# Kernel tuning notes

Hardware: AMD Instinct MI355X
Metric: run time of the kernel (lower is better)

The kernel has to match this reference:

```python
import jax, jax.numpy as jnp
import numpy as np

RADIUS = 0.2
NSAMPLE = 32


def ball_query(radius, nsample, xyz, new_xyz):
    # xyz: (B, N, 3), new_xyz: (B, M, 3) -> idx: (B, M, nsample) int32
    N = xyz.shape[1]
    # squared distances (B, M, N)
    d2 = jnp.sum((new_xyz[:, :, None, :] - xyz[:, None, :, :]) ** 2, axis=-1)
    # key = point index if within radius else N (sentinel); take nsample smallest keys
    key = jnp.where(d2 < radius * radius, jnp.arange(N, dtype=jnp.int32), N)
    neg_top, _ = jax.lax.top_k(-key, nsample)  # ascending keys = earliest in-radius indices
    idx = -neg_top  # (B, M, nsample)
    valid = idx < N
    first = idx[..., :1]
    first = jnp.where(first < N, first, 0)  # if ball empty, fall back to index 0
    return jnp.where(valid, idx, first)


def group_points(features, idx):
    # features: (B, C, N), idx: (B, M, S) -> (B, C, M, S)
    return jax.vmap(lambda f, i: f[:, i])(features, idx)


def setup_inputs() -> dict:
    key = jax.random.key(0)
    k1, k2, k3 = jax.random.split(key, 3)
    B, N, M, C = 4, 16384, 2048, 64
    xyz = jax.random.uniform(k1, (B, N, 3), dtype=jnp.float32)
    new_xyz = jax.random.uniform(k2, (B, M, 3), dtype=jnp.float32)
    features = jax.random.normal(k3, (B, C, N), dtype=jnp.float32)
    return {"xyz": xyz, "new_xyz": new_xyz, "features": features}


def reference(xyz, new_xyz, features):
    idx = ball_query(RADIUS, NSAMPLE, xyz, new_xyz)  # (B, M, S)
    xyz_t = jnp.transpose(xyz, (0, 2, 1))  # (B, 3, N)
    grouped_xyz = group_points(xyz_t, idx)  # (B, 3, M, S)
    grouped_xyz = grouped_xyz - jnp.transpose(new_xyz, (0, 2, 1))[..., None]
    grouped_features = group_points(features, idx)  # (B, C, M, S)
    # use_xyz=True: concat relative coordinates with grouped features
    return jnp.concatenate([grouped_xyz, grouped_features], axis=1)  # (B, 3+C, M, S)
```

## Files before the change

kernel.cpp:

```cpp
#include <hip/hip_runtime.h>


#define WPB 4
constexpr int Bc = 4, Nc = 16384, Mc = 2048, Cc = 64, Sc = 32;

__global__ __launch_bounds__(256) void transpose_kernel(
    const float* __restrict__ feat,
    float* __restrict__ featT)
{
    __shared__ float tile[64][65];
    const int b = blockIdx.y;
    const int nbase = blockIdx.x * 64;
    const int tid = threadIdx.x;
    const int tn = tid & 63;
    const int tq = tid >> 6;
    const float* fb = feat + (size_t)b * Cc * Nc;
    float* ob = featT + (size_t)b * Nc * Cc;
    #pragma unroll
    for (int k = 0; k < 16; ++k) {
        const int c = k * 4 + tq;
        tile[tn][c] = fb[(size_t)c * Nc + nbase + tn];
    }
    __syncthreads();
    #pragma unroll
    for (int k = 0; k < 16; ++k) {
        const int nl = k * 4 + tq;
        ob[(size_t)(nbase + nl) * Cc + tn] = tile[nl][tn];
    }
}

__global__ __launch_bounds__(256) void qg_kernel(
    const float* __restrict__ xyz,
    const float* __restrict__ new_xyz,
    const float* __restrict__ feat,
    const float* __restrict__ featT,
    float* __restrict__ out,
    int useT)
{
#pragma clang fp contract(off)
    const int lane = threadIdx.x & 63;
    const int wv   = threadIdx.x >> 6;
    const int q    = blockIdx.x * WPB + wv;
    const int b    = q >> 11;
    const int m    = q & (Mc - 1);

    __shared__ int sidx[WPB][Sc];

    const float r2 = 0.2f * 0.2f;
    const float* nz = new_xyz + (size_t)(b * Mc + m) * 3;
    const float qx = nz[0], qy = nz[1], qz = nz[2];
    const float* xb = xyz + (size_t)b * Nc * 3;

    int count = 0, firstIdx = 0;
    const unsigned long long lt = (1ull << lane) - 1ull;
    for (int base = 0; base < Nc; base += 256) {
        float px[4], py[4], pz[4];
        #pragma unroll
        for (int u = 0; u < 4; ++u) {
            const float* pp = xb + (size_t)(base + u * 64 + lane) * 3;
            px[u] = pp[0]; py[u] = pp[1]; pz[u] = pp[2];
        }
        #pragma unroll
        for (int u = 0; u < 4; ++u) {
            const float dx = qx - px[u], dy = qy - py[u], dz = qz - pz[u];
            float d2 = dx * dx + dy * dy;
            d2 = d2 + dz * dz;
            const bool in = d2 < r2;
            const unsigned long long mask = __ballot(in);
            if (in) {
                const int slot = count + __popcll(mask & lt);
                if (slot < Sc) sidx[wv][slot] = base + u * 64 + lane;
            }
            if (count == 0 && mask != 0ull)
                firstIdx = base + u * 64 + __builtin_ctzll(mask);
            count += __popcll(mask);
        }
        if (count >= Sc) break;
    }
    {
        const int start = count < Sc ? count : Sc;
        if (start + lane < Sc) sidx[wv][start + lane] = firstIdx;
    }
    asm volatile("s_waitcnt lgkmcnt(0)" ::: "memory");

    const int s     = lane & 31;
    const int chalf = lane >> 5;
    const int myid  = sidx[wv][s];
    float* ob = out + ((size_t)b * 67 * Mc + m) * Sc;

    #pragma unroll
    for (int it = 0; it < 2; ++it) {
        const int c = it * 2 + chalf;
        if (c < 3) {
            const float ctr = (c == 0) ? qx : (c == 1) ? qy : qz;
            ob[(size_t)c * (Mc * Sc) + s] = xb[(size_t)myid * 3 + c] - ctr;
        }
    }

    if (useT) {
        const float* ftb = featT + ((size_t)b * Nc + myid) * Cc;
        #pragma unroll
        for (int it = 0; it < 8; ++it) {
            const int c4 = it * 2 + chalf;
            const float4 v = *(const float4*)(ftb + (size_t)c4 * 4);
            #pragma unroll
            for (int k = 0; k < 4; ++k)
                ob[(size_t)(3 + c4 * 4 + k) * (Mc * Sc) + s] = ((const float*)&v)[k];
        }
    } else {
        const float* fb = feat + (size_t)b * Cc * Nc;
        #pragma unroll
        for (int it = 0; it < 32; ++it) {
            const int c = it * 2 + chalf;
            ob[(size_t)(3 + c) * (Mc * Sc) + s] = fb[(size_t)c * Nc + myid];
        }
    }
}

extern "C" void kernel_launch(void* const* d_in, const int* in_sizes, int n_in,
                              void* d_out, int out_size, void* d_ws, size_t ws_size,
                              hipStream_t stream) {
    const float* xyz     = (const float*)d_in[0];
    const float* new_xyz = (const float*)d_in[1];
    const float* feat    = (const float*)d_in[2];
    float* out           = (float*)d_out;

    const size_t needT = (size_t)Bc * Nc * Cc * sizeof(float);
    float* featT = (float*)d_ws;
    const int useT = (ws_size >= needT) ? 1 : 0;

    if (useT) {
        dim3 g(Nc / 64, Bc);
        hipLaunchKernelGGL(transpose_kernel, g, dim3(256), 0, stream, feat, featT);
    }
    hipLaunchKernelGGL(qg_kernel, dim3((Bc * Mc) / WPB), dim3(256), 0, stream,
                       xyz, new_xyz, feat, featT, out, useT);
}
```

Before: 38.88 us.

## Overlap feature transpose with ball query in one prep kernel, then gather separately

Merges the feature transpose and the ball-query search into a single prep kernel, with different blocks handling each, so the two independent stages can run concurrently instead of back to back. Neighbor indices now go to a global workspace instead of shared memory, and a separate gather kernel reads them and writes the output from the transposed features. The cost is an extra kernel launch and a global round-trip for the index buffer. The shared-memory tile is also allocated in ball-query blocks, which may limit occupancy.

Result: slower. 43.31 us (+11.4%).

```diff
diff --git a/kernel.cpp b/kernel.cpp
--- a/kernel.cpp
+++ b/kernel.cpp
@@ -3,53 +3,52 @@
 
 #define WPB 4
 constexpr int Bc = 4, Nc = 16384, Mc = 2048, Cc = 64, Sc = 32;
+constexpr int TBLOCKS = (Nc / 64) * Bc;
+constexpr int SBLOCKS = (Bc * Mc) / WPB;
 
-__global__ __launch_bounds__(256) void transpose_kernel(
-    const float* __restrict__ feat,
-    float* __restrict__ featT)
-{
-    __shared__ float tile[64][65];
-    const int b = blockIdx.y;
-    const int nbase = blockIdx.x * 64;
-    const int tid = threadIdx.x;
-    const int tn = tid & 63;
-    const int tq = tid >> 6;
-    const float* fb = feat + (size_t)b * Cc * Nc;
-    float* ob = featT + (size_t)b * Nc * Cc;
-    #pragma unroll
-    for (int k = 0; k < 16; ++k) {
-        const int c = k * 4 + tq;
-        tile[tn][c] = fb[(size_t)c * Nc + nbase + tn];
-    }
-    __syncthreads();
-    #pragma unroll
-    for (int k = 0; k < 16; ++k) {
-        const int nl = k * 4 + tq;
-        ob[(size_t)(nbase + nl) * Cc + tn] = tile[nl][tn];
-    }
-}
-
-__global__ __launch_bounds__(256) void qg_kernel(
+__global__ __launch_bounds__(256) void prep_kernel(
     const float* __restrict__ xyz,
     const float* __restrict__ new_xyz,
     const float* __restrict__ feat,
-    const float* __restrict__ featT,
-    float* __restrict__ out,
-    int useT)
+    float* __restrict__ featT,
+    int* __restrict__ idxws)
 {
 #pragma clang fp contract(off)
+    __shared__ float tile[64][65];
+
+    if (blockIdx.x < TBLOCKS) {
+        const int b = blockIdx.x >> 8;
+        const int nbase = (blockIdx.x & 255) * 64;
+        const int tn = threadIdx.x & 63;
+        const int tq = threadIdx.x >> 6;
+        const float* fb = feat + (size_t)b * Cc * Nc;
+        float* ob = featT + (size_t)b * Nc * Cc;
+        #pragma unroll
+        for (int k = 0; k < 16; ++k) {
+            const int c = k * 4 + tq;
+            tile[tn][c] = fb[(size_t)c * Nc + nbase + tn];
+        }
+        __syncthreads();
+        #pragma unroll
+        for (int k = 0; k < 16; ++k) {
+            const int nl = k * 4 + tq;
+            ob[(size_t)(nbase + nl) * Cc + tn] = tile[nl][tn];
+        }
+        return;
+    }
+
+    const int sb   = blockIdx.x - TBLOCKS;
     const int lane = threadIdx.x & 63;
     const int wv   = threadIdx.x >> 6;
-    const int q    = blockIdx.x * WPB + wv;
+    const int q    = sb * WPB + wv;
     const int b    = q >> 11;
     const int m    = q & (Mc - 1);
-
-    __shared__ int sidx[WPB][Sc];
 
     const float r2 = 0.2f * 0.2f;
     const float* nz = new_xyz + (size_t)(b * Mc + m) * 3;
     const float qx = nz[0], qy = nz[1], qz = nz[2];
     const float* xb = xyz + (size_t)b * Nc * 3;
+    int* myidx = idxws + (size_t)q * Sc;
 
     int count = 0, firstIdx = 0;
     const unsigned long long lt = (1ull << lane) - 1ull;
@@ -69,7 +68,7 @@
             const unsigned long long mask = __ballot(in);
             if (in) {
                 const int slot = count + __popcll(mask & lt);
-                if (slot < Sc) sidx[wv][slot] = base + u * 64 + lane;
+                if (slot < Sc) myidx[slot] = base + u * 64 + lane;
             }
             if (count == 0 && mask != 0ull)
                 firstIdx = base + u * 64 + __builtin_ctzll(mask);
@@ -77,17 +76,87 @@
         }
         if (count >= Sc) break;
     }
-    {
-        const int start = count < Sc ? count : Sc;
-        if (start + lane < Sc) sidx[wv][start + lane] = firstIdx;
-    }
-    asm volatile("s_waitcnt lgkmcnt(0)" ::: "memory");
+    const int start = count < Sc ? count : Sc;
+    if (start + lane < Sc) myidx[start + lane] = firstIdx;
+}
 
+__global__ __launch_bounds__(256) void gather_kernel(
+    const float* __restrict__ xyz,
+    const float* __restrict__ new_xyz,
+    const float* __restrict__ featT,
+    const int* __restrict__ idxws,
+    float* __restrict__ out)
+{
+#pragma clang fp contract(off)
+    const int lane  = threadIdx.x & 63;
+    const int wv    = threadIdx.x >> 6;
+    const int q     = blockIdx.x * WPB + wv;
+    const int b     = q >> 11;
+    const int m     = q & (Mc - 1);
     const int s     = lane & 31;
     const int chalf = lane >> 5;
-    const int myid  = sidx[wv][s];
+
+    const int myid = idxws[(size_t)q * Sc + s];
+    const float* nz = new_xyz + (size_t)(b * Mc + m) * 3;
+    const float* xb = xyz + (size_t)b * Nc * 3;
     float* ob = out + ((size_t)b * 67 * Mc + m) * Sc;
 
+    {
+        const float ctr = (chalf == 0) ? nz[0] : nz[1];
+        ob[(size_t)chalf * (Mc * Sc) + s] = xb[(size_t)myid * 3 + chalf] - ctr;
+    }
+    if (chalf == 0)
+        ob[(size_t)2 * (Mc * Sc) + s] = xb[(size_t)myid * 3 + 2] - nz[2];
+
+    const float* ftb = featT + ((size_t)b * Nc + myid) * Cc;
+    #pragma unroll
+    for (int it = 0; it < 8; ++it) {
+        const int c4 = it * 2 + chalf;
+        const float4 v = *(const float4*)(ftb + c4 * 4);
+        #pragma unroll
+        for (int k = 0; k < 4; ++k)
+            ob[(size_t)(3 + c4 * 4 + k) * (Mc * Sc) + s] = ((const float*)&v)[k];
+    }
+}
+
+__global__ __launch_bounds__(256) void qg_fallback_kernel(
+    const float* __restrict__ xyz, const float* __restrict__ new_xyz,
+    const float* __restrict__ feat, float* __restrict__ out)
+{
+#pragma clang fp contract(off)
+    const int lane = threadIdx.x & 63;
+    const int wv   = threadIdx.x >> 6;
+    const int q    = blockIdx.x * WPB + wv;
+    const int b    = q >> 11;
+    const int m    = q & (Mc - 1);
+    __shared__ int sidx[WPB][Sc];
+    const float r2 = 0.2f * 0.2f;
+    const float* nz = new_xyz + (size_t)(b * Mc + m) * 3;
+    const float qx = nz[0], qy = nz[1], qz = nz[2];
+    const float* xb = xyz + (size_t)b * Nc * 3;
+    int count = 0, firstIdx = 0;
+    const unsigned long long lt = (1ull << lane) - 1ull;
+    for (int base = 0; base < Nc; base += 64) {
+        const int i = base + lane;
+        const float px = xb[i * 3], py = xb[i * 3 + 1], pz = xb[i * 3 + 2];
+        const float dx = qx - px, dy = qy - py, dz = qz - pz;
+        float d2 = dx * dx + dy * dy; d2 = d2 + dz * dz;
+        const bool in = d2 < r2;
+        const unsigned long long mask = __ballot(in);
+        if (in) {
+            const int slot = count + __popcll(mask & lt);
+            if (slot < Sc) sidx[wv][slot] = i;
+        }
+        if (count == 0 && mask != 0ull) firstIdx = base + __builtin_ctzll(mask);
+        count += __popcll(mask);
+        if (count >= Sc) break;
+    }
+    const int start = count < Sc ? count : Sc;
+    if (start + lane < Sc) sidx[wv][start + lane] = firstIdx;
+    asm volatile("s_waitcnt lgkmcnt(0)" ::: "memory");
+    const int s = lane & 31, chalf = lane >> 5;
+    const int myid = sidx[wv][s];
+    float* ob = out + ((size_t)b * 67 * Mc + m) * Sc;
     #pragma unroll
     for (int it = 0; it < 2; ++it) {
         const int c = it * 2 + chalf;
@@ -96,24 +165,11 @@
             ob[(size_t)c * (Mc * Sc) + s] = xb[(size_t)myid * 3 + c] - ctr;
         }
     }
-
-    if (useT) {
-        const float* ftb = featT + ((size_t)b * Nc + myid) * Cc;
-        #pragma unroll
-        for (int it = 0; it < 8; ++it) {
-            const int c4 = it * 2 + chalf;
-            const float4 v = *(const float4*)(ftb + (size_t)c4 * 4);
-            #pragma unroll
-            for (int k = 0; k < 4; ++k)
-                ob[(size_t)(3 + c4 * 4 + k) * (Mc * Sc) + s] = ((const float*)&v)[k];
-        }
-    } else {
-        const float* fb = feat + (size_t)b * Cc * Nc;
-        #pragma unroll
-        for (int it = 0; it < 32; ++it) {
-            const int c = it * 2 + chalf;
-            ob[(size_t)(3 + c) * (Mc * Sc) + s] = fb[(size_t)c * Nc + myid];
-        }
+    const float* fb = feat + (size_t)b * Cc * Nc;
+    #pragma unroll
+    for (int it = 0; it < 32; ++it) {
+        const int c = it * 2 + chalf;
+        ob[(size_t)(3 + c) * (Mc * Sc) + s] = fb[(size_t)c * Nc + myid];
     }
 }
 
@@ -125,14 +181,18 @@
     const float* feat    = (const float*)d_in[2];
     float* out           = (float*)d_out;
 
-    const size_t needT = (size_t)Bc * Nc * Cc * sizeof(float);
-    float* featT = (float*)d_ws;
-    const int useT = (ws_size >= needT) ? 1 : 0;
+    const size_t featT_bytes = (size_t)Bc * Nc * Cc * sizeof(float);
+    const size_t idx_bytes   = (size_t)Bc * Mc * Sc * sizeof(int);
 
-    if (useT) {
-        dim3 g(Nc / 64, Bc);
-        hipLaunchKernelGGL(transpose_kernel, g, dim3(256), 0, stream, feat, featT);
+    if (ws_size >= featT_bytes + idx_bytes) {
+        float* featT = (float*)d_ws;
+        int*   idxws = (int*)((char*)d_ws + featT_bytes);
+        hipLaunchKernelGGL(prep_kernel, dim3(TBLOCKS + SBLOCKS), dim3(256), 0, stream,
+                           xyz, new_xyz, feat, featT, idxws);
+        hipLaunchKernelGGL(gather_kernel, dim3(SBLOCKS), dim3(256), 0, stream,
+                           xyz, new_xyz, featT, idxws, out);
+    } else {
+        hipLaunchKernelGGL(qg_fallback_kernel, dim3(SBLOCKS), dim3(256), 0, stream,
+                           xyz, new_xyz, feat, out);
     }
-    hipLaunchKernelGGL(qg_kernel, dim3((Bc * Mc) / WPB), dim3(256), 0, stream,
-                       xyz, new_xyz, feat, featT, out, useT);
 }
```
